# Kernel optimization log

Measured on AMD Instinct MI355X. Metric: run time of the kernel, lower is better.

Reference implementation:

```python
import jax, jax.numpy as jnp
import numpy as np
import math

_DENSE_LOCAL_W = 64
_DYADIC = [96, 128, 192, 256, 384, 512, 768, 1024, 1536]
OFFSETS = sorted(set(range(0, _DENSE_LOCAL_W + 1)) | set(_DYADIC))  # 74 offsets

B, N, D, H = 1, 2048, 1024, 16
HD = D // H


def setup_inputs() -> dict:
    key = jax.random.key(0)
    ks = jax.random.split(key, 8)
    s = 1.0 / math.sqrt(D)
    x = jax.random.normal(ks[0], (B, N, D), dtype=jnp.float32)
    Wqkv = jax.random.uniform(ks[1], (3 * D, D), jnp.float32, -s, s)
    bqkv = jax.random.uniform(ks[2], (3 * D,), jnp.float32, -s, s)
    Wgate = jax.random.uniform(ks[3], (D, D), jnp.float32, -s, s)
    bgate = jax.random.uniform(ks[4], (D,), jnp.float32, -s, s)
    Wout = jax.random.uniform(ks[5], (D, D), jnp.float32, -s, s)
    bout = jax.random.uniform(ks[6], (D,), jnp.float32, -s, s)
    # pos_bias init exactly as in the module: -log(1+delta) * alpha_h, shape (O, H)
    alphas = jnp.linspace(0.2, 2.0, H)
    deltas = jnp.array([math.log(1.0 + d) for d in OFFSETS], dtype=jnp.float32)
    pos_bias = -deltas[:, None] * alphas[None, :]
    offsets = jnp.array(OFFSETS, dtype=jnp.int32)
    return {"x": x, "Wqkv": Wqkv, "bqkv": bqkv, "Wgate": Wgate, "bgate": bgate,
            "Wout": Wout, "bout": bout, "pos_bias": pos_bias, "offsets": offsets}


def reference(x, Wqkv, bqkv, Wgate, bgate, Wout, bout, pos_bias, offsets):
    Bx, Nx, Dx = x.shape
    qkv = x @ Wqkv.T + bqkv                       # (B, N, 3D)
    q, k, v = jnp.split(qkv, 3, axis=-1)
    q = q.reshape(Bx, Nx, H, HD).transpose(0, 2, 1, 3)  # (B, H, N, HD)
    k = k.reshape(Bx, Nx, H, HD).transpose(0, 2, 1, 3)
    v = v.reshape(Bx, Nx, H, HD).transpose(0, 2, 1, 3)
    scale = HD ** -0.5

    # gather shifted K/V: position n attends to n - delta for each fixed offset
    n_idx = jnp.arange(Nx, dtype=jnp.int32)[:, None]      # (N, 1)
    idx = n_idx - offsets[None, :]                        # (N, O)
    valid = idx >= 0                                      # (N, O)
    idx_c = jnp.clip(idx, 0, Nx - 1)
    K_all = k[:, :, idx_c, :]                             # (B, H, N, O, HD)
    V_all = v[:, :, idx_c, :]

    scores = jnp.einsum('bhnd,bhnod->bhno', q, K_all) * scale
    scores = scores + pos_bias.T[None, :, None, :]        # (1, H, 1, O)
    scores = jnp.where(valid[None, None], scores, -jnp.inf)
    alpha = jax.nn.softmax(scores, axis=-1)               # (B, H, N, O)
    out = jnp.einsum('bhno,bhnod->bhnd', alpha, V_all)    # (B, H, N, HD)

    flat = out.transpose(0, 2, 1, 3).reshape(Bx, Nx, Dx)  # (B, N, D)
    gate = jax.nn.sigmoid(x @ Wgate.T + bgate)
    return (flat * gate) @ Wout.T + bout                  # dropout = identity (eval)
```

## Files before the change

### kernel.cpp

```cpp
#include <hip/hip_runtime.h>
#include <hip/hip_bf16.h>

#define SEQ_N 2048
#define DIM   1024
#define NHEAD 16
#define HDIM  64
#define LDQ   4096
#define NOFF  74
#define NDENSE 65
#define NJ    224
#define NT    16
#define PST   232
#define QST   88

typedef __attribute__((ext_vector_type(8)))  __bf16 bv8;
typedef __attribute__((ext_vector_type(4)))  __bf16 bv4;
typedef __attribute__((ext_vector_type(4)))  float  f32x4;
typedef __attribute__((ext_vector_type(16))) float  f32x16;

typedef __attribute__((address_space(3))) void as3_void;
typedef __attribute__((address_space(1))) void as1_void;

__device__ __forceinline__ void async16(const void* g, void* l) {
  __builtin_amdgcn_global_load_lds((as1_void*)(unsigned long long)g,
                                   (as3_void*)l, 16, 0, 0);
}

#define E1 (SEQ_N * DIM)
#define E2 (E1 + 3 * DIM * DIM)
#define E3 (E2 + DIM * DIM)
#define E4 (E3 + DIM * DIM)
__global__ __launch_bounds__(256) void cvt_all(
    const float* __restrict__ x, const float* __restrict__ wqkv,
    const float* __restrict__ wgate, const float* __restrict__ wout,
    __bf16* __restrict__ dst) {
  long i = ((long)blockIdx.x * 256 + threadIdx.x) * 8;
  if (i >= E4) return;
  const float* s; long o;
  if (i < E1)      { s = x;     o = i; }
  else if (i < E2) { s = wqkv;  o = i - E1; }
  else if (i < E3) { s = wgate; o = i - E2; }
  else             { s = wout;  o = i - E3; }
  float4 v0 = *(const float4*)(s + o);
  float4 v1 = *(const float4*)(s + o + 4);
  bv8 ov;
  ov[0] = (__bf16)v0.x; ov[1] = (__bf16)v0.y; ov[2] = (__bf16)v0.z; ov[3] = (__bf16)v0.w;
  ov[4] = (__bf16)v1.x; ov[5] = (__bf16)v1.y; ov[6] = (__bf16)v1.z; ov[7] = (__bf16)v1.w;
  *(bv8*)(dst + i) = ov;
}

template <int BM_, int BN_, int KT_, int WM, int WN, int GX, int GY, typename OutT>
__global__ __launch_bounds__(WM * WN * 64) void gemm_bt2(
    const __bf16* __restrict__ A, const __bf16* __restrict__ B1,
    const __bf16* __restrict__ B2, const float* __restrict__ bias1,
    const float* __restrict__ bias2, int Nsplit,
    OutT* __restrict__ C, int ldc, int K) {
  constexpr int NTHR = WM * WN * 64;
  constexpr int NI  = BM_ / (WM * 32);
  constexpr int NJ_ = BN_ / (WN * 32);
  constexpr int CA = BM_ * KT_ / 8;
  constexpr int CB = BN_ * KT_ / 8;
  constexpr int CT = CA + CB;
  constexpr int CPR = KT_ / 8;
  static_assert(CA % NTHR == 0 && CT % NTHR == 0, "stage divisibility");

  __shared__ __attribute__((aligned(16))) __bf16 smem[2][(BM_ + BN_) * KT_];

  const int tid  = threadIdx.x;
  const int lane = tid & 63;
  const int wave = tid >> 6;
  const int wm = wave / WN, wn = wave % WN;
  const int m31 = lane & 31;
  const int h1  = lane >> 5;
  const int l7  = lane & 7;

  constexpr int NWG = GX * GY;
  const int bid  = blockIdx.y * GX + blockIdx.x;
  const int work = (bid & 7) * (NWG >> 3) + (bid >> 3);
  const int bn0 = (work / GY) * BN_;
  const int bm0 = (work % GY) * BM_;

  const __bf16* Bp;
  const float* biasp;
  if (bn0 < Nsplit) { Bp = B1 + (size_t)bn0 * K;            biasp = bias1 + bn0; }
  else              { Bp = B2 + (size_t)(bn0 - Nsplit) * K; biasp = bias2 + (bn0 - Nsplit); }
  const __bf16* Ap = A + (size_t)bm0 * K;

  f32x16 acc[NI][NJ_] = {};

#define STAGE_STEP(KTOFF, SEL)                                            \
  {                                                                       \
    _Pragma("unroll")                                                     \
    for (int c0 = 0; c0 < CT; c0 += NTHR) {                               \
      int c = c0 + tid;                                                   \
      if (c < CA) {                                                       \
        int rr = c / CPR, qq = c % CPR;                                   \
        int qs = qq ^ (rr & 7);                                           \
        async16(Ap + (size_t)rr * K + (KTOFF) + qs * 8,                   \
                &smem[SEL][0] + c * 8);                                   \
      } else {                                                            \
        int cb = c - CA;                                                  \
        int rr = cb / CPR, qq = cb % CPR;                                 \
        int qs = qq ^ (rr & 7);                                           \
        async16(Bp + (size_t)rr * K + (KTOFF) + qs * 8,                   \
                &smem[SEL][BM_ * KT_] + cb * 8);                          \
      }                                                                   \
    }                                                                     \
  }

  STAGE_STEP(0, 0)
  __syncthreads();

  const int NSTEP = K / KT_;
  int sel = 0;
  for (int t = 0; t < NSTEP; ++t) {
    if (t + 1 < NSTEP) STAGE_STEP((t + 1) * KT_, sel ^ 1)

#pragma unroll
    for (int kk = 0; kk < KT_ / 16; ++kk) {
      const int qs = ((kk * 2 + h1) ^ l7) * 8;
      bv8 af[NI], bfr[NJ_];
#pragma unroll
      for (int i = 0; i < NI; ++i)
        af[i] = *(const bv8*)(&smem[sel][0] +
                              (wm * (BM_ / WM) + i * 32 + m31) * KT_ + qs);
#pragma unroll
      for (int j = 0; j < NJ_; ++j)
        bfr[j] = *(const bv8*)(&smem[sel][BM_ * KT_] +
                               (wn * (BN_ / WN) + j * 32 + m31) * KT_ + qs);
#pragma unroll
      for (int i = 0; i < NI; ++i)
#pragma unroll
        for (int j = 0; j < NJ_; ++j)
          acc[i][j] = __builtin_amdgcn_mfma_f32_32x32x16_bf16(af[i], bfr[j], acc[i][j], 0, 0, 0);
    }

    __syncthreads();
    sel ^= 1;
  }
#undef STAGE_STEP

#pragma unroll
  for (int i = 0; i < NI; ++i) {
#pragma unroll
    for (int j = 0; j < NJ_; ++j) {
      int ccol = wn * (BN_ / WN) + j * 32 + m31;
      float b = biasp[ccol];
#pragma unroll
      for (int reg = 0; reg < 16; ++reg) {
        int row = bm0 + wm * (BM_ / WM) + i * 32 + (reg & 3) + 8 * (reg >> 2) + 4 * h1;
        C[(size_t)row * ldc + bn0 + ccol] = (OutT)(acc[i][j][reg] + b);
      }
    }
  }
}

__global__ __launch_bounds__(256) void attn_mfma(
    const __bf16* __restrict__ qkv,
    const float* __restrict__ pos_bias,
    const int* __restrict__ offsets,
    __bf16* __restrict__ fg) {
  const int n0 = (blockIdx.x >> 4) * NT;
  const int h  = blockIdx.x & 15;
  const int tid = threadIdx.x;
  const int lane = tid & 63;
  const int w = tid >> 6;
  const int fr = lane & 15, fq = lane >> 4;
  const int fr7 = fr & 7;

  __shared__ __attribute__((aligned(16))) __bf16 KVbuf[NJ * HDIM];
  __shared__ __attribute__((aligned(16))) __bf16 Qbuf[NT * QST];
  __shared__ __attribute__((aligned(16))) float  Sbuf[NT][80];
  __shared__ __attribute__((aligned(16))) __bf16 Pd[NT * PST];
  __shared__ float inv_l[NT];

  const int ch = lane & 7;
  const int rowin = lane >> 3;

  if (tid < 128) {
    int ni = tid >> 3, cq = tid & 7;
    bv8 q = *(const bv8*)(qkv + (size_t)(n0 + ni) * LDQ + h * HDIM + cq * 8);
    *(bv8*)(Qbuf + ni * QST + cq * 8) = q;
  }
#pragma unroll
  for (int c0 = 0; c0 < NT * PST / 8; c0 += 256) {
    int c = c0 + tid;
    if (c < NT * PST / 8) *(uint4*)(Pd + c * 8) = make_uint4(0, 0, 0, 0);
  }
  {
    int chs = ch ^ rowin;
#pragma unroll
    for (int it = 0; it < 7; ++it) {
      int jbase = it * 32 + w * 8;
      int j = jbase + rowin;
      int g;
      if (j < 80) g = n0 - 64 + j;
      else { int jj = j - 80; g = n0 - offsets[NDENSE + (jj >> 4)] + (jj & 15); }
      if (g < 0) g = 0;
      async16(qkv + (size_t)g * LDQ + DIM + h * HDIM + chs * 8,
              KVbuf + jbase * HDIM + lane * 8);
    }
  }
  __syncthreads();

  for (int jb = w; jb < 14; jb += 4) {
    f32x4 acc = {};
#pragma unroll
    for (int kk = 0; kk < 2; ++kk) {
      bv8 a = *(const bv8*)(Qbuf + fr * QST + kk * 32 + fq * 8);
      bv8 b = *(const bv8*)(KVbuf + (jb * 16 + fr) * HDIM + ((kk * 4 + fq) ^ fr7) * 8);
      acc = __builtin_amdgcn_mfma_f32_16x16x32_bf16(a, b, acc, 0, 0, 0);
    }
    int j = jb * 16 + fr;
    if (jb < 5) {
      bool gvalid = (n0 - 64 + j) >= 0;
#pragma unroll
      for (int r = 0; r < 4; ++r) {
        int ni = fq * 4 + r;
        int o = ni + 64 - j;
        if (o >= 0 && o < NDENSE)
          Sbuf[ni][o] = gvalid ? acc[r] : -3.0e38f;
      }
    } else {
      int jj = j - 80;
      int s = jj >> 4, tni = jj & 15;
      int r = tni - fq * 4;
      if (r >= 0 && r < 4) {
        bool gvalid = (n0 + tni - offsets[NDENSE + s]) >= 0;
        Sbuf[tni][NDENSE + s] = gvalid ? acc[r] : -3.0e38f;
      }
    }
  }
  __syncthreads();

  {
#pragma unroll
    for (int it = 0; it < 7; ++it) {
      int jbase = it * 32 + w * 8;
      int jv = jbase + (lane >> 5) * 4 + ((lane >> 1) & 3);
      int dv = ((lane >> 3) & 3) * 16 + (lane & 1) * 8;
      int g;
      if (jv < 80) g = n0 - 64 + jv;
      else { int jj = jv - 80; g = n0 - offsets[NDENSE + (jj >> 4)] + (jj & 15); }
      if (g < 0) g = 0;
      async16(qkv + (size_t)g * LDQ + 2 * DIM + h * HDIM + dv,
              KVbuf + jbase * HDIM + lane * 8);
    }
  }

  {
    int t = tid & 15, ni = tid >> 4;
    float sc5[5];
    float m = -3.0e38f;
#pragma unroll
    for (int k = 0; k < 5; ++k) {
      int o = t + k * 16;
      float v = -3.0e38f;
      if (o < NOFF) {
        float raw = Sbuf[ni][o];
        if (raw > -1.0e38f) v = raw * 0.125f + pos_bias[o * NHEAD + h];
      }
      sc5[k] = v;
      m = fmaxf(m, v);
    }
#pragma unroll
    for (int d = 1; d < 16; d <<= 1) m = fmaxf(m, __shfl_xor(m, d));
    float sum = 0.f;
#pragma unroll
    for (int k = 0; k < 5; ++k) {
      int o = t + k * 16;
      if (o < NOFF && sc5[k] > -1.0e38f) {
        float e = __expf(sc5[k] - m);
        sum += e;
        int j = (o < NDENSE) ? (ni + 64 - o) : (80 + (o - NDENSE) * 16 + ni);
        Pd[ni * PST + j] = (__bf16)e;
      }
    }
#pragma unroll
    for (int d = 1; d < 16; d <<= 1) sum += __shfl_xor(sum, d);
    if (t == 0) inv_l[ni] = 1.f / sum;
  }
  __syncthreads();

  {
    const int db = w;
    const unsigned vb0 = (unsigned)(size_t)(as3_void*)KVbuf
                       + fq * 1024 + db * 128 + fr * 8;
    f32x4 acc = {};
#pragma unroll
    for (int kt = 0; kt < 7; ++kt) {
      bv8 a = *(const bv8*)(Pd + fr * PST + kt * 32 + fq * 8);
      bv4 lo, hi;
      asm volatile("ds_read_b64_tr_b16 %0, %2 offset:%3\n\t"
                   "ds_read_b64_tr_b16 %1, %2 offset:%4\n\t"
                   "s_waitcnt lgkmcnt(0)"
                   : "=&v"(lo), "=&v"(hi)
                   : "v"(vb0), "i"(kt * 4096), "i"(kt * 4096 + 512));
      bv8 b;
#pragma unroll
      for (int jj = 0; jj < 4; ++jj) { b[jj] = lo[jj]; b[4 + jj] = hi[jj]; }
      acc = __builtin_amdgcn_mfma_f32_16x16x32_bf16(a, b, acc, 0, 0, 0);
    }
    int d = db * 16 + fr;
#pragma unroll
    for (int r = 0; r < 4; ++r) {
      int ni = fq * 4 + r;
      float o = acc[r] * inv_l[ni];
      float gp = (float)qkv[(size_t)(n0 + ni) * LDQ + 3 * DIM + h * HDIM + d];
      float gate = 1.f / (1.f + __expf(-gp));
      fg[(size_t)(n0 + ni) * DIM + h * HDIM + d] = (__bf16)(o * gate);
    }
  }
}

extern "C" void kernel_launch(void* const* d_in, const int* in_sizes, int n_in,
                              void* d_out, int out_size, void* d_ws, size_t ws_size,
                              hipStream_t stream) {
  const float* x        = (const float*)d_in[0];
  const float* Wqkv     = (const float*)d_in[1];
  const float* bqkv     = (const float*)d_in[2];
  const float* Wgate    = (const float*)d_in[3];
  const float* bgate    = (const float*)d_in[4];
  const float* Wout     = (const float*)d_in[5];
  const float* bout     = (const float*)d_in[6];
  const float* pos_bias = (const float*)d_in[7];
  const int*   offsets  = (const int*)d_in[8];
  float* out = (float*)d_out;

  __bf16* xb       = (__bf16*)d_ws;
  __bf16* Wqkvb    = xb    + (size_t)SEQ_N * DIM;
  __bf16* Wgateb   = Wqkvb + (size_t)3 * DIM * DIM;
  __bf16* Woutb    = Wgateb + (size_t)DIM * DIM;
  __bf16* qkvg     = Woutb + (size_t)DIM * DIM;
  __bf16* flatgate = qkvg + (size_t)SEQ_N * LDQ;

  cvt_all<<<dim3(E4 / 2048), dim3(256), 0, stream>>>(x, Wqkv, Wgate, Wout, xb);

  gemm_bt2<128, 256, 64, 2, 4, 16, 16, __bf16>
      <<<dim3(16, 16), dim3(512), 0, stream>>>(
      xb, Wqkvb, Wgateb, bqkv, bgate, 3 * DIM, qkvg, LDQ, DIM);

  attn_mfma<<<dim3((SEQ_N / NT) * NHEAD), dim3(256), 0, stream>>>(
      qkvg, pos_bias, offsets, flatgate);

  gemm_bt2<64, 128, 64, 2, 2, 8, 32, float>
      <<<dim3(8, 32), dim3(256), 0, stream>>>(
      flatgate, Woutb, Woutb, bout, bout, DIM, out, DIM, DIM);
}
```

Before: 143.9 us.

## Fuse all stages into one cooperative persistent kernel with grid syncs

Replaces the four separate launches (convert, QKV+gate GEMM, attention, output GEMM) with a single cooperative kernel of 256 blocks × 512 threads that runs each phase in turn and separates them with grid.sync(). The attention phase runs two 256-thread tiles per block on split LDS halves, and the output GEMM now uses 8 waves per block instead of 4. This is meant to remove inter-kernel launch gaps and tail idle time, at the cost of grid-barrier overhead and fixed occupancy (256 blocks, 96KB LDS). The old multi-launch path is kept as a fallback if the cooperative launch fails.

Measured after the change: 265.3 us. 1.84x slower.

```diff
diff --git a/kernel.cpp b/kernel.cpp
--- a/kernel.cpp
+++ b/kernel.cpp
@@ -1,5 +1,8 @@
 #include <hip/hip_runtime.h>
 #include <hip/hip_bf16.h>
+#include <hip/hip_cooperative_groups.h>
+
+namespace cg = cooperative_groups;
 
 #define SEQ_N 2048
 #define DIM   1024
@@ -30,6 +33,324 @@
 #define E2 (E1 + 3 * DIM * DIM)
 #define E3 (E2 + DIM * DIM)
 #define E4 (E3 + DIM * DIM)
+
+template <int BM_, int BN_, int KT_, int WM, int WN, int GX, int GY, typename OutT>
+__device__ __forceinline__ void gemm_body(
+    char* ldsb, int bid, int tid,
+    const __bf16* __restrict__ A, const __bf16* __restrict__ B1,
+    const __bf16* __restrict__ B2, const float* __restrict__ bias1,
+    const float* __restrict__ bias2, int Nsplit,
+    OutT* __restrict__ C, int ldc, int K) {
+  constexpr int NTHR = WM * WN * 64;
+  constexpr int NI  = BM_ / (WM * 32);
+  constexpr int NJ_ = BN_ / (WN * 32);
+  constexpr int CA = BM_ * KT_ / 8;
+  constexpr int CB = BN_ * KT_ / 8;
+  constexpr int CT = CA + CB;
+  constexpr int CPR = KT_ / 8;
+  constexpr int BUF = (BM_ + BN_) * KT_;
+  static_assert(CA % NTHR == 0 && CT % NTHR == 0, "stage divisibility");
+
+  __bf16* smem = (__bf16*)ldsb;
+
+  const int lane = tid & 63;
+  const int wave = tid >> 6;
+  const int wm = wave / WN, wn = wave % WN;
+  const int m31 = lane & 31;
+  const int h1  = lane >> 5;
+  const int l7  = lane & 7;
+
+  constexpr int NWG = GX * GY;
+  const int work = (bid & 7) * (NWG >> 3) + (bid >> 3);
+  const int bn0 = (work / GY) * BN_;
+  const int bm0 = (work % GY) * BM_;
+
+  const __bf16* Bp;
+  const float* biasp;
+  if (bn0 < Nsplit) { Bp = B1 + (size_t)bn0 * K;            biasp = bias1 + bn0; }
+  else              { Bp = B2 + (size_t)(bn0 - Nsplit) * K; biasp = bias2 + (bn0 - Nsplit); }
+  const __bf16* Ap = A + (size_t)bm0 * K;
+
+  f32x16 acc[NI][NJ_] = {};
+
+  auto stage = [&](int ktoff, int sel_) {
+#pragma unroll
+    for (int c0 = 0; c0 < CT; c0 += NTHR) {
+      int c = c0 + tid;
+      if (c < CA) {
+        int rr = c / CPR, qq = c % CPR;
+        int qs = qq ^ (rr & 7);
+        async16(Ap + (size_t)rr * K + ktoff + qs * 8, smem + sel_ * BUF + c * 8);
+      } else {
+        int cb = c - CA;
+        int rr = cb / CPR, qq = cb % CPR;
+        int qs = qq ^ (rr & 7);
+        async16(Bp + (size_t)rr * K + ktoff + qs * 8,
+                smem + sel_ * BUF + BM_ * KT_ + cb * 8);
+      }
+    }
+  };
+
+  stage(0, 0);
+  __syncthreads();
+
+  const int NSTEP = K / KT_;
+  int sel = 0;
+  for (int t = 0; t < NSTEP; ++t) {
+    if (t + 1 < NSTEP) stage((t + 1) * KT_, sel ^ 1);
+
+#pragma unroll
+    for (int kk = 0; kk < KT_ / 16; ++kk) {
+      const int qs = ((kk * 2 + h1) ^ l7) * 8;
+      bv8 af[NI], bfr[NJ_];
+#pragma unroll
+      for (int i = 0; i < NI; ++i)
+        af[i] = *(const bv8*)(smem + sel * BUF +
+                              (wm * (BM_ / WM) + i * 32 + m31) * KT_ + qs);
+#pragma unroll
+      for (int j = 0; j < NJ_; ++j)
+        bfr[j] = *(const bv8*)(smem + sel * BUF + BM_ * KT_ +
+                               (wn * (BN_ / WN) + j * 32 + m31) * KT_ + qs);
+#pragma unroll
+      for (int i = 0; i < NI; ++i)
+#pragma unroll
+        for (int j = 0; j < NJ_; ++j)
+          acc[i][j] = __builtin_amdgcn_mfma_f32_32x32x16_bf16(af[i], bfr[j], acc[i][j], 0, 0, 0);
+    }
+
+    __syncthreads();
+    sel ^= 1;
+  }
+
+#pragma unroll
+  for (int i = 0; i < NI; ++i) {
+#pragma unroll
+    for (int j = 0; j < NJ_; ++j) {
+      int ccol = wn * (BN_ / WN) + j * 32 + m31;
+      float b = biasp[ccol];
+#pragma unroll
+      for (int reg = 0; reg < 16; ++reg) {
+        int row = bm0 + wm * (BM_ / WM) + i * 32 + (reg & 3) + 8 * (reg >> 2) + 4 * h1;
+        C[(size_t)row * ldc + bn0 + ccol] = (OutT)(acc[i][j][reg] + b);
+      }
+    }
+  }
+}
+
+__device__ __forceinline__ void attn_tile(
+    const __bf16* __restrict__ qkv, const float* __restrict__ pos_bias,
+    const int* __restrict__ offsets, __bf16* __restrict__ fg,
+    char* ldsh, int n0, int h, int tid2) {
+  __bf16* KVbuf = (__bf16*)ldsh;
+  __bf16* Qbuf  = (__bf16*)(ldsh + 28672);
+  float (*Sbuf)[80] = (float(*)[80])(ldsh + 31488);
+  __bf16* Pd    = (__bf16*)(ldsh + 36608);
+  float* inv_l  = (float*)(ldsh + 44032);
+
+  const int lane = tid2 & 63;
+  const int w = tid2 >> 6;
+  const int fr = lane & 15, fq = lane >> 4;
+  const int fr7 = fr & 7;
+  const int ch = lane & 7;
+  const int rowin = lane >> 3;
+
+  if (tid2 < 128) {
+    int ni = tid2 >> 3, cq = tid2 & 7;
+    bv8 q = *(const bv8*)(qkv + (size_t)(n0 + ni) * LDQ + h * HDIM + cq * 8);
+    *(bv8*)(Qbuf + ni * QST + cq * 8) = q;
+  }
+#pragma unroll
+  for (int c0 = 0; c0 < NT * PST / 8; c0 += 256) {
+    int c = c0 + tid2;
+    if (c < NT * PST / 8) *(uint4*)(Pd + c * 8) = make_uint4(0, 0, 0, 0);
+  }
+  {
+    int chs = ch ^ rowin;
+#pragma unroll
+    for (int it = 0; it < 7; ++it) {
+      int jbase = it * 32 + w * 8;
+      int j = jbase + rowin;
+      int g;
+      if (j < 80) g = n0 - 64 + j;
+      else { int jj = j - 80; g = n0 - offsets[NDENSE + (jj >> 4)] + (jj & 15); }
+      if (g < 0) g = 0;
+      async16(qkv + (size_t)g * LDQ + DIM + h * HDIM + chs * 8,
+              KVbuf + jbase * HDIM + lane * 8);
+    }
+  }
+  __syncthreads();
+
+  for (int jb = w; jb < 14; jb += 4) {
+    f32x4 acc = {};
+#pragma unroll
+    for (int kk = 0; kk < 2; ++kk) {
+      bv8 a = *(const bv8*)(Qbuf + fr * QST + kk * 32 + fq * 8);
+      bv8 b = *(const bv8*)(KVbuf + (jb * 16 + fr) * HDIM + ((kk * 4 + fq) ^ fr7) * 8);
+      acc = __builtin_amdgcn_mfma_f32_16x16x32_bf16(a, b, acc, 0, 0, 0);
+    }
+    int j = jb * 16 + fr;
+    if (jb < 5) {
+      bool gvalid = (n0 - 64 + j) >= 0;
+#pragma unroll
+      for (int r = 0; r < 4; ++r) {
+        int ni = fq * 4 + r;
+        int o = ni + 64 - j;
+        if (o >= 0 && o < NDENSE)
+          Sbuf[ni][o] = gvalid ? acc[r] : -3.0e38f;
+      }
+    } else {
+      int jj = j - 80;
+      int s = jj >> 4, tni = jj & 15;
+      int r = tni - fq * 4;
+      if (r >= 0 && r < 4) {
+        bool gvalid = (n0 + tni - offsets[NDENSE + s]) >= 0;
+        Sbuf[tni][NDENSE + s] = gvalid ? acc[r] : -3.0e38f;
+      }
+    }
+  }
+  __syncthreads();
+
+  {
+#pragma unroll
+    for (int it = 0; it < 7; ++it) {
+      int jbase = it * 32 + w * 8;
+      int jv = jbase + (lane >> 5) * 4 + ((lane >> 1) & 3);
+      int dv = ((lane >> 3) & 3) * 16 + (lane & 1) * 8;
+      int g;
+      if (jv < 80) g = n0 - 64 + jv;
+      else { int jj = jv - 80; g = n0 - offsets[NDENSE + (jj >> 4)] + (jj & 15); }
+      if (g < 0) g = 0;
+      async16(qkv + (size_t)g * LDQ + 2 * DIM + h * HDIM + dv,
+              KVbuf + jbase * HDIM + lane * 8);
+    }
+  }
+
+  {
+    int t = tid2 & 15, ni = tid2 >> 4;
+    float sc5[5];
+    float m = -3.0e38f;
+#pragma unroll
+    for (int k = 0; k < 5; ++k) {
+      int o = t + k * 16;
+      float v = -3.0e38f;
+      if (o < NOFF) {
+        float raw = Sbuf[ni][o];
+        if (raw > -1.0e38f) v = raw * 0.125f + pos_bias[o * NHEAD + h];
+      }
+      sc5[k] = v;
+      m = fmaxf(m, v);
+    }
+#pragma unroll
+    for (int d = 1; d < 16; d <<= 1) m = fmaxf(m, __shfl_xor(m, d));
+    float sum = 0.f;
+#pragma unroll
+    for (int k = 0; k < 5; ++k) {
+      int o = t + k * 16;
+      if (o < NOFF && sc5[k] > -1.0e38f) {
+        float e = __expf(sc5[k] - m);
+        sum += e;
+        int j = (o < NDENSE) ? (ni + 64 - o) : (80 + (o - NDENSE) * 16 + ni);
+        Pd[ni * PST + j] = (__bf16)e;
+      }
+    }
+#pragma unroll
+    for (int d = 1; d < 16; d <<= 1) sum += __shfl_xor(sum, d);
+    if (t == 0) inv_l[ni] = 1.f / sum;
+  }
+  __syncthreads();
+
+  {
+    const int db = w;
+    const unsigned vb0 = (unsigned)(size_t)(as3_void*)KVbuf
+                       + fq * 1024 + db * 128 + fr * 8;
+    f32x4 acc = {};
+#pragma unroll
+    for (int kt = 0; kt < 7; ++kt) {
+      bv8 a = *(const bv8*)(Pd + fr * PST + kt * 32 + fq * 8);
+      bv4 lo, hi;
+      asm volatile("ds_read_b64_tr_b16 %0, %2 offset:%3\n\t"
+                   "ds_read_b64_tr_b16 %1, %2 offset:%4\n\t"
+                   "s_waitcnt lgkmcnt(0)"
+                   : "=&v"(lo), "=&v"(hi)
+                   : "v"(vb0), "i"(kt * 4096), "i"(kt * 4096 + 512));
+      bv8 b;
+#pragma unroll
+      for (int jj = 0; jj < 4; ++jj) { b[jj] = lo[jj]; b[4 + jj] = hi[jj]; }
+      acc = __builtin_amdgcn_mfma_f32_16x16x32_bf16(a, b, acc, 0, 0, 0);
+    }
+    int d = db * 16 + fr;
+#pragma unroll
+    for (int r = 0; r < 4; ++r) {
+      int ni = fq * 4 + r;
+      float o = acc[r] * inv_l[ni];
+      float gp = (float)qkv[(size_t)(n0 + ni) * LDQ + 3 * DIM + h * HDIM + d];
+      float gate = 1.f / (1.f + __expf(-gp));
+      fg[(size_t)(n0 + ni) * DIM + h * HDIM + d] = (__bf16)(o * gate);
+    }
+  }
+}
+
+__global__ __launch_bounds__(512, 2) void fused_all(
+    const float* __restrict__ x, const float* __restrict__ Wqkv,
+    const float* __restrict__ bqkv, const float* __restrict__ Wgate,
+    const float* __restrict__ bgate, const float* __restrict__ Wout,
+    const float* __restrict__ bout, const float* __restrict__ pos_bias,
+    const int* __restrict__ offsets, float* __restrict__ out,
+    __bf16* __restrict__ ws) {
+  __shared__ __attribute__((aligned(16))) char lds[98304];
+  const int tid = threadIdx.x;
+  const int bid = blockIdx.x;
+
+  __bf16* xb       = ws;
+  __bf16* Wqkvb    = xb    + (size_t)SEQ_N * DIM;
+  __bf16* Wgateb   = Wqkvb + (size_t)3 * DIM * DIM;
+  __bf16* Woutb    = Wgateb + (size_t)DIM * DIM;
+  __bf16* qkvg     = Woutb + (size_t)DIM * DIM;
+  __bf16* flatgate = qkvg  + (size_t)SEQ_N * LDQ;
+
+  cg::grid_group grid = cg::this_grid();
+
+  {
+    const int gt = bid * 512 + tid;
+#pragma unroll
+    for (int it = 0; it < 7; ++it) {
+      long i = ((long)(it * 131072 + gt)) * 8;
+      const float* s; long o;
+      if (i < E1)      { s = x;     o = i; }
+      else if (i < E2) { s = Wqkv;  o = i - E1; }
+      else if (i < E3) { s = Wgate; o = i - E2; }
+      else             { s = Wout;  o = i - E3; }
+      float4 v0 = *(const float4*)(s + o);
+      float4 v1 = *(const float4*)(s + o + 4);
+      bv8 ov;
+      ov[0] = (__bf16)v0.x; ov[1] = (__bf16)v0.y; ov[2] = (__bf16)v0.z; ov[3] = (__bf16)v0.w;
+      ov[4] = (__bf16)v1.x; ov[5] = (__bf16)v1.y; ov[6] = (__bf16)v1.z; ov[7] = (__bf16)v1.w;
+      *(bv8*)(ws + i) = ov;
+    }
+  }
+  grid.sync();
+
+  gemm_body<128, 256, 64, 2, 4, 16, 16, __bf16>(
+      lds, bid, tid, xb, Wqkvb, Wgateb, bqkv, bgate, 3 * DIM, qkvg, LDQ, DIM);
+  grid.sync();
+
+  {
+    const int half = tid >> 8;
+    const int tid2 = tid & 255;
+    char* ldsh = lds + half * 49152;
+    for (int r = 0; r < 4; ++r) {
+      int widx = bid * 8 + r * 2 + half;
+      attn_tile(qkvg, pos_bias, offsets, flatgate, ldsh,
+                (widx >> 4) * NT, widx & 15, tid2);
+      __syncthreads();
+    }
+  }
+  grid.sync();
+
+  gemm_body<64, 128, 64, 2, 4, 8, 32, float>(
+      lds, bid, tid, flatgate, Woutb, Woutb, bout, bout, DIM, out, DIM, DIM);
+}
+
 __global__ __launch_bounds__(256) void cvt_all(
     const float* __restrict__ x, const float* __restrict__ wqkv,
     const float* __restrict__ wgate, const float* __restrict__ wout,
@@ -55,262 +376,18 @@
     const __bf16* __restrict__ B2, const float* __restrict__ bias1,
     const float* __restrict__ bias2, int Nsplit,
     OutT* __restrict__ C, int ldc, int K) {
-  constexpr int NTHR = WM * WN * 64;
-  constexpr int NI  = BM_ / (WM * 32);
-  constexpr int NJ_ = BN_ / (WN * 32);
-  constexpr int CA = BM_ * KT_ / 8;
-  constexpr int CB = BN_ * KT_ / 8;
-  constexpr int CT = CA + CB;
-  constexpr int CPR = KT_ / 8;
-  static_assert(CA % NTHR == 0 && CT % NTHR == 0, "stage divisibility");
-
-  __shared__ __attribute__((aligned(16))) __bf16 smem[2][(BM_ + BN_) * KT_];
-
-  const int tid  = threadIdx.x;
-  const int lane = tid & 63;
-  const int wave = tid >> 6;
-  const int wm = wave / WN, wn = wave % WN;
-  const int m31 = lane & 31;
-  const int h1  = lane >> 5;
-  const int l7  = lane & 7;
-
-  constexpr int NWG = GX * GY;
-  const int bid  = blockIdx.y * GX + blockIdx.x;
-  const int work = (bid & 7) * (NWG >> 3) + (bid >> 3);
-  const int bn0 = (work / GY) * BN_;
-  const int bm0 = (work % GY) * BM_;
-
-  const __bf16* Bp;
-  const float* biasp;
-  if (bn0 < Nsplit) { Bp = B1 + (size_t)bn0 * K;            biasp = bias1 + bn0; }
-  else              { Bp = B2 + (size_t)(bn0 - Nsplit) * K; biasp = bias2 + (bn0 - Nsplit); }
-  const __bf16* Ap = A + (size_t)bm0 * K;
-
-  f32x16 acc[NI][NJ_] = {};
-
-#define STAGE_STEP(KTOFF, SEL)                                            \
-  {                                                                       \
-    _Pragma("unroll")                                                     \
-    for (int c0 = 0; c0 < CT; c0 += NTHR) {                               \
-      int c = c0 + tid;                                                   \
-      if (c < CA) {                                                       \
-        int rr = c / CPR, qq = c % CPR;                                   \
-        int qs = qq ^ (rr & 7);                                           \
-        async16(Ap + (size_t)rr * K + (KTOFF) + qs * 8,                   \
-                &smem[SEL][0] + c * 8);                                   \
-      } else {                                                            \
-        int cb = c - CA;                                                  \
-        int rr = cb / CPR, qq = cb % CPR;                                 \
-        int qs = qq ^ (rr & 7);                                           \
-        async16(Bp + (size_t)rr * K + (KTOFF) + qs * 8,                   \
-                &smem[SEL][BM_ * KT_] + cb * 8);                          \
-      }                                                                   \
-    }                                                                     \
-  }
-
-  STAGE_STEP(0, 0)
-  __syncthreads();
-
-  const int NSTEP = K / KT_;
-  int sel = 0;
-  for (int t = 0; t < NSTEP; ++t) {
-    if (t + 1 < NSTEP) STAGE_STEP((t + 1) * KT_, sel ^ 1)
-
-#pragma unroll
-    for (int kk = 0; kk < KT_ / 16; ++kk) {
-      const int qs = ((kk * 2 + h1) ^ l7) * 8;
-      bv8 af[NI], bfr[NJ_];
-#pragma unroll
-      for (int i = 0; i < NI; ++i)
-        af[i] = *(const bv8*)(&smem[sel][0] +
-                              (wm * (BM_ / WM) + i * 32 + m31) * KT_ + qs);
-#pragma unroll
-      for (int j = 0; j < NJ_; ++j)
-        bfr[j] = *(const bv8*)(&smem[sel][BM_ * KT_] +
-                               (wn * (BN_ / WN) + j * 32 + m31) * KT_ + qs);
-#pragma unroll
-      for (int i = 0; i < NI; ++i)
-#pragma unroll
-        for (int j = 0; j < NJ_; ++j)
-          acc[i][j] = __builtin_amdgcn_mfma_f32_32x32x16_bf16(af[i], bfr[j], acc[i][j], 0, 0, 0);
-    }
-
-    __syncthreads();
-    sel ^= 1;
-  }
-#undef STAGE_STEP
-
-#pragma unroll
-  for (int i = 0; i < NI; ++i) {
-#pragma unroll
-    for (int j = 0; j < NJ_; ++j) {
-      int ccol = wn * (BN_ / WN) + j * 32 + m31;
-      float b = biasp[ccol];
-#pragma unroll
-      for (int reg = 0; reg < 16; ++reg) {
-        int row = bm0 + wm * (BM_ / WM) + i * 32 + (reg & 3) + 8 * (reg >> 2) + 4 * h1;
-        C[(size_t)row * ldc + bn0 + ccol] = (OutT)(acc[i][j][reg] + b);
-      }
-    }
-  }
+  __shared__ __attribute__((aligned(16))) char lds[2 * (BM_ + BN_) * KT_ * 2];
+  gemm_body<BM_, BN_, KT_, WM, WN, GX, GY, OutT>(
+      lds, blockIdx.y * GX + blockIdx.x, threadIdx.x,
+      A, B1, B2, bias1, bias2, Nsplit, C, ldc, K);
 }
 
 __global__ __launch_bounds__(256) void attn_mfma(
-    const __bf16* __restrict__ qkv,
-    const float* __restrict__ pos_bias,
-    const int* __restrict__ offsets,
-    __bf16* __restrict__ fg) {
-  const int n0 = (blockIdx.x >> 4) * NT;
-  const int h  = blockIdx.x & 15;
-  const int tid = threadIdx.x;
-  const int lane = tid & 63;
-  const int w = tid >> 6;
-  const int fr = lane & 15, fq = lane >> 4;
-  const int fr7 = fr & 7;
-
-  __shared__ __attribute__((aligned(16))) __bf16 KVbuf[NJ * HDIM];
-  __shared__ __attribute__((aligned(16))) __bf16 Qbuf[NT * QST];
-  __shared__ __attribute__((aligned(16))) float  Sbuf[NT][80];
-  __shared__ __attribute__((aligned(16))) __bf16 Pd[NT * PST];
-  __shared__ float inv_l[NT];
-
-  const int ch = lane & 7;
-  const int rowin = lane >> 3;
-
-  if (tid < 128) {
-    int ni = tid >> 3, cq = tid & 7;
-    bv8 q = *(const bv8*)(qkv + (size_t)(n0 + ni) * LDQ + h * HDIM + cq * 8);
-    *(bv8*)(Qbuf + ni * QST + cq * 8) = q;
-  }
-#pragma unroll
-  for (int c0 = 0; c0 < NT * PST / 8; c0 += 256) {
-    int c = c0 + tid;
-    if (c < NT * PST / 8) *(uint4*)(Pd + c * 8) = make_uint4(0, 0, 0, 0);
-  }
-  {
-    int chs = ch ^ rowin;
-#pragma unroll
-    for (int it = 0; it < 7; ++it) {
-      int jbase = it * 32 + w * 8;
-      int j = jbase + rowin;
-      int g;
-      if (j < 80) g = n0 - 64 + j;
-      else { int jj = j - 80; g = n0 - offsets[NDENSE + (jj >> 4)] + (jj & 15); }
-      if (g < 0) g = 0;
-      async16(qkv + (size_t)g * LDQ + DIM + h * HDIM + chs * 8,
-              KVbuf + jbase * HDIM + lane * 8);
-    }
-  }
-  __syncthreads();
-
-  for (int jb = w; jb < 14; jb += 4) {
-    f32x4 acc = {};
-#pragma unroll
-    for (int kk = 0; kk < 2; ++kk) {
-      bv8 a = *(const bv8*)(Qbuf + fr * QST + kk * 32 + fq * 8);
-      bv8 b = *(const bv8*)(KVbuf + (jb * 16 + fr) * HDIM + ((kk * 4 + fq) ^ fr7) * 8);
-      acc = __builtin_amdgcn_mfma_f32_16x16x32_bf16(a, b, acc, 0, 0, 0);
-    }
-    int j = jb * 16 + fr;
-    if (jb < 5) {
-      bool gvalid = (n0 - 64 + j) >= 0;
-#pragma unroll
-      for (int r = 0; r < 4; ++r) {
-        int ni = fq * 4 + r;
-        int o = ni + 64 - j;
-        if (o >= 0 && o < NDENSE)
-          Sbuf[ni][o] = gvalid ? acc[r] : -3.0e38f;
-      }
-    } else {
-      int jj = j - 80;
-      int s = jj >> 4, tni = jj & 15;
-      int r = tni - fq * 4;
-      if (r >= 0 && r < 4) {
-        bool gvalid = (n0 + tni - offsets[NDENSE + s]) >= 0;
-        Sbuf[tni][NDENSE + s] = gvalid ? acc[r] : -3.0e38f;
-      }
-    }
-  }
-  __syncthreads();
-
-  {
-#pragma unroll
-    for (int it = 0; it < 7; ++it) {
-      int jbase = it * 32 + w * 8;
-      int jv = jbase + (lane >> 5) * 4 + ((lane >> 1) & 3);
-      int dv = ((lane >> 3) & 3) * 16 + (lane & 1) * 8;
-      int g;
-      if (jv < 80) g = n0 - 64 + jv;
-      else { int jj = jv - 80; g = n0 - offsets[NDENSE + (jj >> 4)] + (jj & 15); }
-      if (g < 0) g = 0;
-      async16(qkv + (size_t)g * LDQ + 2 * DIM + h * HDIM + dv,
-              KVbuf + jbase * HDIM + lane * 8);
-    }
-  }
-
-  {
-    int t = tid & 15, ni = tid >> 4;
-    float sc5[5];
-    float m = -3.0e38f;
-#pragma unroll
-    for (int k = 0; k < 5; ++k) {
-      int o = t + k * 16;
-      float v = -3.0e38f;
-      if (o < NOFF) {
-        float raw = Sbuf[ni][o];
-        if (raw > -1.0e38f) v = raw * 0.125f + pos_bias[o * NHEAD + h];
-      }
-      sc5[k] = v;
-      m = fmaxf(m, v);
-    }
-#pragma unroll
-    for (int d = 1; d < 16; d <<= 1) m = fmaxf(m, __shfl_xor(m, d));
-    float sum = 0.f;
-#pragma unroll
-    for (int k = 0; k < 5; ++k) {
-      int o = t + k * 16;
-      if (o < NOFF && sc5[k] > -1.0e38f) {
-        float e = __expf(sc5[k] - m);
-        sum += e;
-        int j = (o < NDENSE) ? (ni + 64 - o) : (80 + (o - NDENSE) * 16 + ni);
-        Pd[ni * PST + j] = (__bf16)e;
-      }
-    }
-#pragma unroll
-    for (int d = 1; d < 16; d <<= 1) sum += __shfl_xor(sum, d);
-    if (t == 0) inv_l[ni] = 1.f / sum;
-  }
-  __syncthreads();
-
-  {
-    const int db = w;
-    const unsigned vb0 = (unsigned)(size_t)(as3_void*)KVbuf
-                       + fq * 1024 + db * 128 + fr * 8;
-    f32x4 acc = {};
-#pragma unroll
-    for (int kt = 0; kt < 7; ++kt) {
-      bv8 a = *(const bv8*)(Pd + fr * PST + kt * 32 + fq * 8);
-      bv4 lo, hi;
-      asm volatile("ds_read_b64_tr_b16 %0, %2 offset:%3\n\t"
-                   "ds_read_b64_tr_b16 %1, %2 offset:%4\n\t"
-                   "s_waitcnt lgkmcnt(0)"
-                   : "=&v"(lo), "=&v"(hi)
-                   : "v"(vb0), "i"(kt * 4096), "i"(kt * 4096 + 512));
-      bv8 b;
-#pragma unroll
-      for (int jj = 0; jj < 4; ++jj) { b[jj] = lo[jj]; b[4 + jj] = hi[jj]; }
-      acc = __builtin_amdgcn_mfma_f32_16x16x32_bf16(a, b, acc, 0, 0, 0);
-    }
-    int d = db * 16 + fr;
-#pragma unroll
-    for (int r = 0; r < 4; ++r) {
-      int ni = fq * 4 + r;
-      float o = acc[r] * inv_l[ni];
-      float gp = (float)qkv[(size_t)(n0 + ni) * LDQ + 3 * DIM + h * HDIM + d];
-      float gate = 1.f / (1.f + __expf(-gp));
-      fg[(size_t)(n0 + ni) * DIM + h * HDIM + d] = (__bf16)(o * gate);
-    }
-  }
+    const __bf16* __restrict__ qkv, const float* __restrict__ pos_bias,
+    const int* __restrict__ offsets, __bf16* __restrict__ fg) {
+  __shared__ __attribute__((aligned(16))) char lds[44096];
+  attn_tile(qkv, pos_bias, offsets, fg, lds,
+            (blockIdx.x >> 4) * NT, blockIdx.x & 15, threadIdx.x);
 }
 
 extern "C" void kernel_launch(void* const* d_in, const int* in_sizes, int n_in,
@@ -326,24 +403,29 @@
   const float* pos_bias = (const float*)d_in[7];
   const int*   offsets  = (const int*)d_in[8];
   float* out = (float*)d_out;
-
-  __bf16* xb       = (__bf16*)d_ws;
-  __bf16* Wqkvb    = xb    + (size_t)SEQ_N * DIM;
-  __bf16* Wgateb   = Wqkvb + (size_t)3 * DIM * DIM;
-  __bf16* Woutb    = Wgateb + (size_t)DIM * DIM;
-  __bf16* qkvg     = Woutb + (size_t)DIM * DIM;
-  __bf16* flatgate = qkvg + (size_t)SEQ_N * LDQ;
-
-  cvt_all<<<dim3(E4 / 2048), dim3(256), 0, stream>>>(x, Wqkv, Wgate, Wout, xb);
-
-  gemm_bt2<128, 256, 64, 2, 4, 16, 16, __bf16>
-      <<<dim3(16, 16), dim3(512), 0, stream>>>(
-      xb, Wqkvb, Wgateb, bqkv, bgate, 3 * DIM, qkvg, LDQ, DIM);
-
-  attn_mfma<<<dim3((SEQ_N / NT) * NHEAD), dim3(256), 0, stream>>>(
-      qkvg, pos_bias, offsets, flatgate);
-
-  gemm_bt2<64, 128, 64, 2, 2, 8, 32, float>
-      <<<dim3(8, 32), dim3(256), 0, stream>>>(
-      flatgate, Woutb, Woutb, bout, bout, DIM, out, DIM, DIM);
-}
+  __bf16* wsb = (__bf16*)d_ws;
+
+  void* args[] = {(void*)&x, (void*)&Wqkv, (void*)&bqkv, (void*)&Wgate,
+                  (void*)&bgate, (void*)&Wout, (void*)&bout, (void*)&pos_bias,
+                  (void*)&offsets, (void*)&out, (void*)&wsb};
+  hipError_t e = hipLaunchCooperativeKernel((const void*)fused_all,
+                                            dim3(256), dim3(512), args, 0, stream);
+  if (e != hipSuccess) {
+    __bf16* xb       = wsb;
+    __bf16* Wqkvb    = xb    + (size_t)SEQ_N * DIM;
+    __bf16* Wgateb   = Wqkvb + (size_t)3 * DIM * DIM;
+    __bf16* Woutb    = Wgateb + (size_t)DIM * DIM;
+    __bf16* qkvg     = Woutb + (size_t)DIM * DIM;
+    __bf16* flatgate = qkvg  + (size_t)SEQ_N * LDQ;
+
+    cvt_all<<<dim3(E4 / 2048), dim3(256), 0, stream>>>(x, Wqkv, Wgate, Wout, xb);
+    gemm_bt2<128, 256, 64, 2, 4, 16, 16, __bf16>
+        <<<dim3(16, 16), dim3(512), 0, stream>>>(
+        xb, Wqkvb, Wgateb, bqkv, bgate, 3 * DIM, qkvg, LDQ, DIM);
+    attn_mfma<<<dim3((SEQ_N / NT) * NHEAD), dim3(256), 0, stream>>>(
+        qkvg, pos_bias, offsets, flatgate);
+    gemm_bt2<64, 128, 64, 2, 2, 8, 32, float>
+        <<<dim3(8, 32), dim3(256), 0, stream>>>(
+        flatgate, Woutb, Woutb, bout, bout, DIM, out, DIM, DIM);
+  }
+}
```

## Fuse fp32-to-bf16 conversion into GEMM tile loading, drop separate convert kernel

Applied to the files above, without the earlier changes.

Removes the standalone conversion kernel that cast x and all weights to bf16 in workspace. The GEMMs now load fp32 tiles into registers during compute, convert them to bf16, and write them to shared memory after the MFMA loop (register-staged prefetch). This saves one launch and the extra write and read of the bf16 copies. In exchange, each GEMM block reads twice the bytes from global memory, and since tiles are reused across blocks, the conversion work is repeated. It also uses more registers and gives up the async global-to-LDS path for those operands.

After: 148.1 us. 2.9% more time.

```diff
diff --git a/kernel.cpp b/kernel.cpp
--- a/kernel.cpp
+++ b/kernel.cpp
@@ -26,33 +26,11 @@
                                    (as3_void*)l, 16, 0, 0);
 }
 
-#define E1 (SEQ_N * DIM)
-#define E2 (E1 + 3 * DIM * DIM)
-#define E3 (E2 + DIM * DIM)
-#define E4 (E3 + DIM * DIM)
-__global__ __launch_bounds__(256) void cvt_all(
-    const float* __restrict__ x, const float* __restrict__ wqkv,
-    const float* __restrict__ wgate, const float* __restrict__ wout,
-    __bf16* __restrict__ dst) {
-  long i = ((long)blockIdx.x * 256 + threadIdx.x) * 8;
-  if (i >= E4) return;
-  const float* s; long o;
-  if (i < E1)      { s = x;     o = i; }
-  else if (i < E2) { s = wqkv;  o = i - E1; }
-  else if (i < E3) { s = wgate; o = i - E2; }
-  else             { s = wout;  o = i - E3; }
-  float4 v0 = *(const float4*)(s + o);
-  float4 v1 = *(const float4*)(s + o + 4);
-  bv8 ov;
-  ov[0] = (__bf16)v0.x; ov[1] = (__bf16)v0.y; ov[2] = (__bf16)v0.z; ov[3] = (__bf16)v0.w;
-  ov[4] = (__bf16)v1.x; ov[5] = (__bf16)v1.y; ov[6] = (__bf16)v1.z; ov[7] = (__bf16)v1.w;
-  *(bv8*)(dst + i) = ov;
-}
-
-template <int BM_, int BN_, int KT_, int WM, int WN, int GX, int GY, typename OutT>
-__global__ __launch_bounds__(WM * WN * 64) void gemm_bt2(
-    const __bf16* __restrict__ A, const __bf16* __restrict__ B1,
-    const __bf16* __restrict__ B2, const float* __restrict__ bias1,
+template <int BM_, int BN_, int KT_, int WM, int WN, int GX, int GY,
+          bool AF32, typename OutT>
+__global__ __launch_bounds__(WM * WN * 64) void gemm_cvt(
+    const void* __restrict__ Av, const float* __restrict__ B1,
+    const float* __restrict__ B2, const float* __restrict__ bias1,
     const float* __restrict__ bias2, int Nsplit,
     OutT* __restrict__ C, int ldc, int K) {
   constexpr int NTHR = WM * WN * 64;
@@ -60,11 +38,13 @@
   constexpr int NJ_ = BN_ / (WN * 32);
   constexpr int CA = BM_ * KT_ / 8;
   constexpr int CB = BN_ * KT_ / 8;
-  constexpr int CT = CA + CB;
+  constexpr int NCA = CA / NTHR;
+  constexpr int NCB = CB / NTHR;
   constexpr int CPR = KT_ / 8;
-  static_assert(CA % NTHR == 0 && CT % NTHR == 0, "stage divisibility");
-
-  __shared__ __attribute__((aligned(16))) __bf16 smem[2][(BM_ + BN_) * KT_];
+  constexpr int BUF = (BM_ + BN_) * KT_;
+  static_assert(CA % NTHR == 0 && CB % NTHR == 0, "stage divisibility");
+
+  __shared__ __attribute__((aligned(16))) __bf16 smem[2 * BUF];
 
   const int tid  = threadIdx.x;
   const int lane = tid & 63;
@@ -80,41 +60,83 @@
   const int bn0 = (work / GY) * BN_;
   const int bm0 = (work % GY) * BM_;
 
-  const __bf16* Bp;
+  const float* Bp;
   const float* biasp;
   if (bn0 < Nsplit) { Bp = B1 + (size_t)bn0 * K;            biasp = bias1 + bn0; }
   else              { Bp = B2 + (size_t)(bn0 - Nsplit) * K; biasp = bias2 + (bn0 - Nsplit); }
-  const __bf16* Ap = A + (size_t)bm0 * K;
+  const float*  Afp = (const float*)Av  + (AF32 ? (size_t)bm0 * K : 0);
+  const __bf16* Abf = (const __bf16*)Av + (AF32 ? 0 : (size_t)bm0 * K);
 
   f32x16 acc[NI][NJ_] = {};
 
-#define STAGE_STEP(KTOFF, SEL)                                            \
-  {                                                                       \
-    _Pragma("unroll")                                                     \
-    for (int c0 = 0; c0 < CT; c0 += NTHR) {                               \
-      int c = c0 + tid;                                                   \
-      if (c < CA) {                                                       \
-        int rr = c / CPR, qq = c % CPR;                                   \
-        int qs = qq ^ (rr & 7);                                           \
-        async16(Ap + (size_t)rr * K + (KTOFF) + qs * 8,                   \
-                &smem[SEL][0] + c * 8);                                   \
-      } else {                                                            \
-        int cb = c - CA;                                                  \
-        int rr = cb / CPR, qq = cb % CPR;                                 \
-        int qs = qq ^ (rr & 7);                                           \
-        async16(Bp + (size_t)rr * K + (KTOFF) + qs * 8,                   \
-                &smem[SEL][BM_ * KT_] + cb * 8);                          \
-      }                                                                   \
-    }                                                                     \
-  }
-
-  STAGE_STEP(0, 0)
+  float4 ra[AF32 ? NCA : 1][2];
+  float4 rb[NCB][2];
+
+  auto load_step = [&](int ktoff, int sel_) {
+    if constexpr (AF32) {
+#pragma unroll
+      for (int ci = 0; ci < NCA; ++ci) {
+        int c = ci * NTHR + tid;
+        int rr = c / CPR, qq = c % CPR;
+        int qs = qq ^ (rr & 7);
+        const float* g = Afp + (size_t)rr * K + ktoff + qs * 8;
+        ra[ci][0] = *(const float4*)g;
+        ra[ci][1] = *(const float4*)(g + 4);
+      }
+    } else {
+#pragma unroll
+      for (int ci = 0; ci < NCA; ++ci) {
+        int c = ci * NTHR + tid;
+        int rr = c / CPR, qq = c % CPR;
+        int qs = qq ^ (rr & 7);
+        async16(Abf + (size_t)rr * K + ktoff + qs * 8,
+                smem + sel_ * BUF + c * 8);
+      }
+    }
+#pragma unroll
+    for (int ci = 0; ci < NCB; ++ci) {
+      int cb = ci * NTHR + tid;
+      int rr = cb / CPR, qq = cb % CPR;
+      int qs = qq ^ (rr & 7);
+      const float* g = Bp + (size_t)rr * K + ktoff + qs * 8;
+      rb[ci][0] = *(const float4*)g;
+      rb[ci][1] = *(const float4*)(g + 4);
+    }
+  };
+
+  auto write_step = [&](int sel_) {
+    if constexpr (AF32) {
+#pragma unroll
+      for (int ci = 0; ci < NCA; ++ci) {
+        int c = ci * NTHR + tid;
+        bv8 ov;
+        ov[0] = (__bf16)ra[ci][0].x; ov[1] = (__bf16)ra[ci][0].y;
+        ov[2] = (__bf16)ra[ci][0].z; ov[3] = (__bf16)ra[ci][0].w;
+        ov[4] = (__bf16)ra[ci][1].x; ov[5] = (__bf16)ra[ci][1].y;
+        ov[6] = (__bf16)ra[ci][1].z; ov[7] = (__bf16)ra[ci][1].w;
+        *(bv8*)(smem + sel_ * BUF + c * 8) = ov;
+      }
+    }
+#pragma unroll
+    for (int ci = 0; ci < NCB; ++ci) {
+      int cb = ci * NTHR + tid;
+      bv8 ov;
+      ov[0] = (__bf16)rb[ci][0].x; ov[1] = (__bf16)rb[ci][0].y;
+      ov[2] = (__bf16)rb[ci][0].z; ov[3] = (__bf16)rb[ci][0].w;
+      ov[4] = (__bf16)rb[ci][1].x; ov[5] = (__bf16)rb[ci][1].y;
+      ov[6] = (__bf16)rb[ci][1].z; ov[7] = (__bf16)rb[ci][1].w;
+      *(bv8*)(smem + sel_ * BUF + BM_ * KT_ + cb * 8) = ov;
+    }
+  };
+
+  load_step(0, 0);
+  write_step(0);
   __syncthreads();
 
   const int NSTEP = K / KT_;
   int sel = 0;
   for (int t = 0; t < NSTEP; ++t) {
-    if (t + 1 < NSTEP) STAGE_STEP((t + 1) * KT_, sel ^ 1)
+    if (t + 1 < NSTEP) load_step((t + 1) * KT_, sel ^ 1);
 
 #pragma unroll
     for (int kk = 0; kk < KT_ / 16; ++kk) {
@@ -122,11 +144,11 @@
       bv8 af[NI], bfr[NJ_];
 #pragma unroll
       for (int i = 0; i < NI; ++i)
-        af[i] = *(const bv8*)(&smem[sel][0] +
+        af[i] = *(const bv8*)(smem + sel * BUF +
                               (wm * (BM_ / WM) + i * 32 + m31) * KT_ + qs);
 #pragma unroll
       for (int j = 0; j < NJ_; ++j)
-        bfr[j] = *(const bv8*)(&smem[sel][BM_ * KT_] +
+        bfr[j] = *(const bv8*)(smem + sel * BUF + BM_ * KT_ +
                                (wn * (BN_ / WN) + j * 32 + m31) * KT_ + qs);
 #pragma unroll
       for (int i = 0; i < NI; ++i)
@@ -135,10 +157,11 @@
           acc[i][j] = __builtin_amdgcn_mfma_f32_32x32x16_bf16(af[i], bfr[j], acc[i][j], 0, 0, 0);
     }
 
+    if (t + 1 < NSTEP) write_step(sel ^ 1);
+
     __syncthreads();
     sel ^= 1;
   }
-#undef STAGE_STEP
 
 #pragma unroll
   for (int i = 0; i < NI; ++i) {
@@ -327,23 +350,17 @@
   const int*   offsets  = (const int*)d_in[8];
   float* out = (float*)d_out;
 
-  __bf16* xb       = (__bf16*)d_ws;
-  __bf16* Wqkvb    = xb    + (size_t)SEQ_N * DIM;
-  __bf16* Wgateb   = Wqkvb + (size_t)3 * DIM * DIM;
-  __bf16* Woutb    = Wgateb + (size_t)DIM * DIM;
-  __bf16* qkvg     = Woutb + (size_t)DIM * DIM;
+  __bf16* qkvg     = (__bf16*)d_ws;
   __bf16* flatgate = qkvg + (size_t)SEQ_N * LDQ;
 
-  cvt_all<<<dim3(E4 / 2048), dim3(256), 0, stream>>>(x, Wqkv, Wgate, Wout, xb);
-
-  gemm_bt2<128, 256, 64, 2, 4, 16, 16, __bf16>
+  gemm_cvt<128, 256, 64, 2, 4, 16, 16, true, __bf16>
       <<<dim3(16, 16), dim3(512), 0, stream>>>(
-      xb, Wqkvb, Wgateb, bqkv, bgate, 3 * DIM, qkvg, LDQ, DIM);
+      (const void*)x, Wqkv, Wgate, bqkv, bgate, 3 * DIM, qkvg, LDQ, DIM);
 
   attn_mfma<<<dim3((SEQ_N / NT) * NHEAD), dim3(256), 0, stream>>>(
       qkvg, pos_bias, offsets, flatgate);
 
-  gemm_bt2<64, 128, 64, 2, 2, 8, 32, float>
+  gemm_cvt<64, 128, 64, 2, 2, 8, 32, false, float>
       <<<dim3(8, 32), dim3(256), 0, stream>>>(
-      flatgate, Woutb, Woutb, bout, bout, DIM, out, DIM, DIM);
+      (const void*)flatgate, Wout, Wout, bout, bout, DIM, out, DIM, DIM);
 }
```

## Triple-buffer GEMM K-tiles with two-ahead async prefetch and vmcnt waits

Applied to the files above, without the earlier changes.

Both GEMMs move from a double-buffered shared-memory pipeline to a three-buffer ring. Tiles are prefetched two steps ahead, and each step needs only a partial s_waitcnt vmcnt plus one barrier instead of a full __syncthreads, so global-to-LDS loads for the next tiles can stay in flight while MFMAs run. The inner loop is also reordered to loop over (i,j) outer and k inner, with s_setprio raised around the MFMA bursts. In exchange, LDS use grows by half, which can lower occupancy for the smaller GEMM. The reorder also re-reads A and B fragments from LDS for every (i,j) pair, adding LDS traffic.

New measurement: 149.5 us. +3.9%, slower.

```diff
diff --git a/kernel.cpp b/kernel.cpp
--- a/kernel.cpp
+++ b/kernel.cpp
@@ -50,7 +50,7 @@
 }
 
 template <int BM_, int BN_, int KT_, int WM, int WN, int GX, int GY, typename OutT>
-__global__ __launch_bounds__(WM * WN * 64) void gemm_bt2(
+__global__ __launch_bounds__(WM * WN * 64) void gemm_p(
     const __bf16* __restrict__ A, const __bf16* __restrict__ B1,
     const __bf16* __restrict__ B2, const float* __restrict__ bias1,
     const float* __restrict__ bias2, int Nsplit,
@@ -62,9 +62,11 @@
   constexpr int CB = BN_ * KT_ / 8;
   constexpr int CT = CA + CB;
   constexpr int CPR = KT_ / 8;
+  constexpr int TBUF = (BM_ + BN_) * KT_;
   static_assert(CA % NTHR == 0 && CT % NTHR == 0, "stage divisibility");
-
-  __shared__ __attribute__((aligned(16))) __bf16 smem[2][(BM_ + BN_) * KT_];
+  static_assert(CT / NTHR == 6, "vmcnt(6) assumes 6 async16/wave/tile");
+
+  __shared__ __attribute__((aligned(16))) __bf16 smem[3 * TBUF];
 
   const int tid  = threadIdx.x;
   const int lane = tid & 63;
@@ -88,57 +90,62 @@
 
   f32x16 acc[NI][NJ_] = {};
 
-#define STAGE_STEP(KTOFF, SEL)                                            \
-  {                                                                       \
-    _Pragma("unroll")                                                     \
-    for (int c0 = 0; c0 < CT; c0 += NTHR) {                               \
-      int c = c0 + tid;                                                   \
-      if (c < CA) {                                                       \
-        int rr = c / CPR, qq = c % CPR;                                   \
-        int qs = qq ^ (rr & 7);                                           \
-        async16(Ap + (size_t)rr * K + (KTOFF) + qs * 8,                   \
-                &smem[SEL][0] + c * 8);                                   \
-      } else {                                                            \
-        int cb = c - CA;                                                  \
-        int rr = cb / CPR, qq = cb % CPR;                                 \
-        int qs = qq ^ (rr & 7);                                           \
-        async16(Bp + (size_t)rr * K + (KTOFF) + qs * 8,                   \
-                &smem[SEL][BM_ * KT_] + cb * 8);                          \
-      }                                                                   \
-    }                                                                     \
-  }
-
-  STAGE_STEP(0, 0)
-  __syncthreads();
+  auto stage = [&](int ktoff, int buf) {
+#pragma unroll
+    for (int c0 = 0; c0 < CT; c0 += NTHR) {
+      int c = c0 + tid;
+      if (c < CA) {
+        int rr = c / CPR, qq = c % CPR;
+        int qs = qq ^ (rr & 7);
+        async16(Ap + (size_t)rr * K + ktoff + qs * 8, smem + buf * TBUF + c * 8);
+      } else {
+        int cb = c - CA;
+        int rr = cb / CPR, qq = cb % CPR;
+        int qs = qq ^ (rr & 7);
+        async16(Bp + (size_t)rr * K + ktoff + qs * 8,
+                smem + buf * TBUF + BM_ * KT_ + cb * 8);
+      }
+    }
+  };
 
   const int NSTEP = K / KT_;
-  int sel = 0;
+  stage(0, 0);
+  stage(KT_, 1);
+  asm volatile("s_waitcnt vmcnt(6)" ::: "memory");
+  __builtin_amdgcn_s_barrier();
+  __builtin_amdgcn_sched_barrier(0);
+
   for (int t = 0; t < NSTEP; ++t) {
-    if (t + 1 < NSTEP) STAGE_STEP((t + 1) * KT_, sel ^ 1)
-
-#pragma unroll
-    for (int kk = 0; kk < KT_ / 16; ++kk) {
-      const int qs = ((kk * 2 + h1) ^ l7) * 8;
-      bv8 af[NI], bfr[NJ_];
-#pragma unroll
-      for (int i = 0; i < NI; ++i)
-        af[i] = *(const bv8*)(&smem[sel][0] +
-                              (wm * (BM_ / WM) + i * 32 + m31) * KT_ + qs);
-#pragma unroll
-      for (int j = 0; j < NJ_; ++j)
-        bfr[j] = *(const bv8*)(&smem[sel][BM_ * KT_] +
-                               (wn * (BN_ / WN) + j * 32 + m31) * KT_ + qs);
-#pragma unroll
-      for (int i = 0; i < NI; ++i)
-#pragma unroll
-        for (int j = 0; j < NJ_; ++j)
-          acc[i][j] = __builtin_amdgcn_mfma_f32_32x32x16_bf16(af[i], bfr[j], acc[i][j], 0, 0, 0);
-    }
-
-    __syncthreads();
-    sel ^= 1;
-  }
-#undef STAGE_STEP
+    const int cb = t % 3;
+    if (t + 2 < NSTEP) stage((t + 2) * KT_, (t + 2) % 3);
+
+    const __bf16* As = smem + cb * TBUF;
+    const __bf16* Bs = smem + cb * TBUF + BM_ * KT_;
+#pragma unroll
+    for (int i = 0; i < NI; ++i)
+#pragma unroll
+      for (int j = 0; j < NJ_; ++j) {
+        bv8 af[KT_ / 16], bf[KT_ / 16];
+#pragma unroll
+        for (int kk = 0; kk < KT_ / 16; ++kk) {
+          const int qs = ((kk * 2 + h1) ^ l7) * 8;
+          af[kk] = *(const bv8*)(As + (wm * (BM_ / WM) + i * 32 + m31) * KT_ + qs);
+          bf[kk] = *(const bv8*)(Bs + (wn * (BN_ / WN) + j * 32 + m31) * KT_ + qs);
+        }
+        __builtin_amdgcn_s_setprio(1);
+#pragma unroll
+        for (int kk = 0; kk < KT_ / 16; ++kk)
+          acc[i][j] = __builtin_amdgcn_mfma_f32_32x32x16_bf16(af[kk], bf[kk], acc[i][j], 0, 0, 0);
+        __builtin_amdgcn_s_setprio(0);
+      }
+
+    if (t + 1 < NSTEP) {
+      if (t + 2 < NSTEP) asm volatile("s_waitcnt vmcnt(6)" ::: "memory");
+      else               asm volatile("s_waitcnt vmcnt(0)" ::: "memory");
+      __builtin_amdgcn_s_barrier();
+      __builtin_amdgcn_sched_barrier(0);
+    }
+  }
 
 #pragma unroll
   for (int i = 0; i < NI; ++i) {
@@ -336,14 +343,14 @@
 
   cvt_all<<<dim3(E4 / 2048), dim3(256), 0, stream>>>(x, Wqkv, Wgate, Wout, xb);
 
-  gemm_bt2<128, 256, 64, 2, 4, 16, 16, __bf16>
+  gemm_p<128, 256, 64, 2, 4, 16, 16, __bf16>
       <<<dim3(16, 16), dim3(512), 0, stream>>>(
       xb, Wqkvb, Wgateb, bqkv, bgate, 3 * DIM, qkvg, LDQ, DIM);
 
   attn_mfma<<<dim3((SEQ_N / NT) * NHEAD), dim3(256), 0, stream>>>(
       qkvg, pos_bias, offsets, flatgate);
 
-  gemm_bt2<64, 128, 64, 2, 2, 8, 32, float>
+  gemm_p<64, 128, 64, 2, 2, 8, 32, float>
       <<<dim3(8, 32), dim3(256), 0, stream>>>(
       flatgate, Woutb, Woutb, bout, bout, DIM, out, DIM, DIM);
 }
```
